# Optimization experiments

Hardware: AMD Instinct MI355X
Metric: run time of the kernel (lower is better)

The kernel has to match this reference:

```python
import jax, jax.numpy as jnp
import numpy as np

N_GRID = 512
B = 4
NUM_VIEWS = 4
EPS = 1e-6


def _build_mesh(n):
    # grid mesh with |v| in (0, 0.9] so log(|v|/(1-|v|)) is finite and sign(v) != 0
    xs = np.linspace(-0.9, 0.9, n, dtype=np.float32)  # 512 points -> no exact zero
    X, Y = np.meshgrid(xs, xs, indexing='ij')
    Z = 0.1 * np.abs(np.sin(3.0 * X) * np.cos(3.0 * Y)) + 0.01
    V = np.stack([X, Y, Z], -1).reshape(-1, 3).astype(np.float32)
    idx = np.arange(n * n).reshape(n, n)
    v00, v01 = idx[:-1, :-1].ravel(), idx[:-1, 1:].ravel()
    v10, v11 = idx[1:, :-1].ravel(), idx[1:, 1:].ravel()
    f1 = np.stack([v00, v10, v01], -1)
    f2 = np.stack([v10, v11, v01], -1)
    F = np.concatenate([f1, f2], 0).astype(np.int64)
    return V, F


def _topology(F, nv):
    # per-face edges + the opposite vertex of each edge within its face
    e = np.concatenate([F[:, [0, 1]], F[:, [1, 2]], F[:, [2, 0]]], 0)
    opp = np.concatenate([F[:, 2], F[:, 0], F[:, 1]], 0)
    key = np.sort(e, axis=1)
    uniq, inv, counts = np.unique(key, axis=0, return_inverse=True, return_counts=True)
    # LaplacianLoss: unique neighbor pairs (matrix assignment dedups), both directions
    src = np.concatenate([uniq[:, 0], uniq[:, 1]]).astype(np.int32)
    dst = np.concatenate([uniq[:, 1], uniq[:, 0]]).astype(np.int32)
    deg = np.bincount(dst, minlength=nv).astype(np.int32)
    # FlattenLoss: edges shared by exactly two faces -> (v0,v1) edge, (v2,v3) opposite verts
    order = np.argsort(inv, kind='stable')
    starts = np.searchsorted(inv[order], np.arange(len(uniq)))
    m2 = counts == 2
    i1 = order[starts[m2]]
    i2 = order[starts[m2] + 1]
    v0s = uniq[m2, 0].astype(np.int32)
    v1s = uniq[m2, 1].astype(np.int32)
    v2s = opp[i1].astype(np.int32)
    v3s = opp[i2].astype(np.int32)
    return src, dst, deg, v0s, v1s, v2s, v3s


def setup_inputs() -> dict:
    key = jax.random.key(0)
    k1, k2, k3 = jax.random.split(key, 3)
    Vt, F = _build_mesh(N_GRID)
    nv = Vt.shape[0]
    src, dst, deg, v0s, v1s, v2s, v3s = _topology(F, nv)
    return {
        'displace': jax.random.normal(k1, (B, nv, 3), jnp.float32) * 0.1,
        'center': jax.random.normal(k2, (B, 1, 3), jnp.float32) * 0.1,
        'texture': jax.random.uniform(k3, (B, nv, 3), jnp.float32),
        'template_vertices': jnp.asarray(Vt)[None],  # [1, V, 3]
        'lap_src': jnp.asarray(src),
        'lap_dst': jnp.asarray(dst),
        'deg': jnp.asarray(deg),
        'v0s': jnp.asarray(v0s),
        'v1s': jnp.asarray(v1s),
        'v2s': jnp.asarray(v2s),
        'v3s': jnp.asarray(v3s),
        'num_views': NUM_VIEWS,
    }


def reference(displace, center, texture, template_vertices, lap_src, lap_dst, deg,
              v0s, v1s, v2s, v3s, num_views):
    nv = template_vertices.shape[1]
    tv = template_vertices  # [1, V, 3]
    # vertex warp (elementwise)
    base = jnp.log(jnp.abs(tv) / (1.0 - jnp.abs(tv)))
    centroid = jnp.tanh(center)  # [B, 1, 3]
    v = jax.nn.sigmoid(base + displace) * jnp.sign(tv)  # [B, V, 3]
    v = jax.nn.relu(v) * (1.0 - centroid) - jax.nn.relu(-v) * (centroid + 1.0)
    v = v + centroid

    # uniform Laplacian loss: Lx = x - mean(neighbors); sum of squares per batch, mean over batch
    inv_deg = 1.0 / deg.astype(v.dtype)

    def lap_one(x):  # x: [V, 3]
        nbr = jax.ops.segment_sum(x[lap_src], lap_dst, num_segments=nv)
        return x - nbr * inv_deg[:, None]

    lx = jax.vmap(lap_one)(v)
    lap_loss = jnp.mean(jnp.sum(lx * lx, axis=(1, 2)))

    # flatten loss over face pairs sharing an edge
    p0, p1, p2, p3 = v[:, v0s], v[:, v1s], v[:, v2s], v[:, v3s]  # [B, P, 3]
    a1 = p1 - p0
    a1l2 = jnp.sum(a1 * a1, -1)
    a1l1 = jnp.sqrt(a1l2 + EPS)

    def _comp(b):
        bl2 = jnp.sum(b * b, -1)
        bl1 = jnp.sqrt(bl2 + EPS)
        ab = jnp.sum(a1 * b, -1)
        cos = ab / (a1l1 * bl1 + EPS)
        sin = jnp.sqrt(1.0 - cos * cos + EPS)
        cb = b - a1 * (ab / (a1l2 + EPS))[..., None]
        return cb, bl1 * sin

    cb1, l1 = _comp(p2 - p0)
    cb2, l2 = _comp(p3 - p0)
    cos = jnp.sum(cb1 * cb2, -1) / (l1 * l2 + EPS)
    flat_loss = jnp.mean(jnp.sum((cos + 1.0) ** 2, axis=1))

    # torch repeat(1, numViews, 1).reshape(numViews*B, V, 3) == tile then reshape
    b = v.shape[0]
    verts_out = jnp.tile(v, (1, num_views, 1)).reshape(num_views * b, nv, 3)
    tex_out = jnp.tile(texture, (1, num_views, 1)).reshape(num_views * b, nv, 3)
    return verts_out, tex_out, lap_loss, flat_loss
```

## Files before the change

kernel.cpp:

```cpp
#include <hip/hip_runtime.h>

#define NGRID 512
#define NV (NGRID * NGRID)
#define NB 4
#define NVIEWS 4
#define FEPS 1e-6f
#define TR 2
#define LDS_ROWS (TR + 2)
#define ROWF (NGRID * 3)
#define LDSF (LDS_ROWS * ROWF)

typedef float fvec4 __attribute__((ext_vector_type(4)));

static constexpr size_t NVF3 = (size_t)NV * 3;
static constexpr size_t VERTS_FLOATS = (size_t)NVIEWS * NB * NVF3;
static constexpr size_t LAP_OFF = 2 * VERTS_FLOATS;
static constexpr size_t FLAT_OFF = LAP_OFF + 1;

__device__ __forceinline__ float frcp(float x)  { return __builtin_amdgcn_rcpf(x); }
__device__ __forceinline__ float fsqrt_(float x){ return __builtin_amdgcn_sqrtf(x); }

__global__ void init_losses(float* __restrict__ out) {
    if (threadIdx.x == 0) {
        out[LAP_OFF] = 0.0f;
        out[FLAT_OFF] = 0.0f;
    }
}

__device__ __forceinline__ float3 ldsP(const float* __restrict__ vs, int lr, int c) {
    const int o = lr * ROWF + c * 3;
    return make_float3(vs[o], vs[o + 1], vs[o + 2]);
}

__device__ __forceinline__ float edge_val(float3 p0, float3 p1, float3 p2, float3 p3) {
    const float a1x = p1.x - p0.x, a1y = p1.y - p0.y, a1z = p1.z - p0.z;
    const float a1l2 = a1x * a1x + a1y * a1y + a1z * a1z;
    const float a1l1 = fsqrt_(a1l2 + FEPS);
    const float inv_a1l2 = frcp(a1l2 + FEPS);

    const float b1x = p2.x - p0.x, b1y = p2.y - p0.y, b1z = p2.z - p0.z;
    const float b1l2 = b1x * b1x + b1y * b1y + b1z * b1z;
    const float b1l1 = fsqrt_(b1l2 + FEPS);
    const float ab1 = a1x * b1x + a1y * b1y + a1z * b1z;
    const float cos1 = ab1 * frcp(a1l1 * b1l1 + FEPS);
    const float sin1 = fsqrt_(1.0f - cos1 * cos1 + FEPS);
    const float f1 = ab1 * inv_a1l2;
    const float cb1x = b1x - a1x * f1, cb1y = b1y - a1y * f1, cb1z = b1z - a1z * f1;
    const float l1 = b1l1 * sin1;

    const float b2x = p3.x - p0.x, b2y = p3.y - p0.y, b2z = p3.z - p0.z;
    const float b2l2 = b2x * b2x + b2y * b2y + b2z * b2z;
    const float b2l1 = fsqrt_(b2l2 + FEPS);
    const float ab2 = a1x * b2x + a1y * b2y + a1z * b2z;
    const float cos2 = ab2 * frcp(a1l1 * b2l1 + FEPS);
    const float sin2 = fsqrt_(1.0f - cos2 * cos2 + FEPS);
    const float f2 = ab2 * inv_a1l2;
    const float cb2x = b2x - a1x * f2, cb2y = b2y - a1y * f2, cb2z = b2z - a1z * f2;
    const float l2 = b2l1 * sin2;

    const float cosd = (cb1x * cb2x + cb1y * cb2y + cb1z * cb2z) * frcp(l1 * l2 + FEPS);
    const float t = cosd + 1.0f;
    return t * t;
}

__global__ __launch_bounds__(256) void mesh_fused_kernel(
    const float* __restrict__ disp, const float* __restrict__ center,
    const float* __restrict__ tex, const float* __restrict__ tv,
    float* __restrict__ out)
{
    __shared__ float vs[LDSF];
    const int tid = threadIdx.x;
    const int b = blockIdx.y;
    const int R0 = blockIdx.x * TR;

    const float c0 = tanhf(center[b * 3 + 0]);
    const float c1 = tanhf(center[b * 3 + 1]);
    const float c2 = tanhf(center[b * 3 + 2]);
    const float carr[3] = {c0, c1, c2};

    {
        const fvec4* __restrict__ tv4 = (const fvec4*)tv;
        const fvec4* __restrict__ d4p = (const fvec4*)(disp + (size_t)b * NVF3);
        fvec4* __restrict__ vs4 = (fvec4*)vs;
        const int start4 = (R0 - 1) * (ROWF / 4);
#pragma unroll
        for (int ss = 0; ss < LDSF / 4 / 256; ++ss) {
            const int ff4 = ss * 256 + tid;
            const int g4 = start4 + ff4;
            if (g4 < 0 || g4 >= (int)(NVF3 / 4)) continue;
            const fvec4 t = tv4[g4];
            const fvec4 d = d4p[g4];
            fvec4 vr;
            int comp = ff4 % 3;
#pragma unroll
            for (int l = 0; l < 4; ++l) {
                const float tvl = t[l];
                const float s = fabsf(tvl);
                const float sgn = (tvl > 0.0f) ? 1.0f : -1.0f;
                const float e = __expf(-d[l]);
                const float sigma = s * frcp(fmaf(1.0f - s, e, s));
                const float c = carr[comp];
                vr[l] = fmaf(sigma, sgn - c, c);
                comp = (comp == 2) ? 0 : comp + 1;
            }
            vs4[ff4] = vr;
        }
    }
    __syncthreads();

    {
        const fvec4* __restrict__ vs4 = (const fvec4*)vs;
        const fvec4* __restrict__ t4p = (const fvec4*)(tex + (size_t)b * NVF3);
        fvec4* __restrict__ out4 = (fvec4*)out;
        const size_t blk4 = NVF3 / 4;
        const int tile_base4 = R0 * (ROWF / 4);
#pragma unroll
        for (int qq = 0; qq < TR * ROWF / 4 / 256; ++qq) {
            const int q = qq * 256 + tid;
            const fvec4 vo = vs4[ROWF / 4 + q];
            const fvec4 tx = __builtin_nontemporal_load(&t4p[tile_base4 + q]);
            const size_t pos4 = (size_t)tile_base4 + q;
#pragma unroll
            for (int view = 0; view < NVIEWS; ++view) {
                const size_t base = (size_t)(b * NVIEWS + view) * blk4;
                __builtin_nontemporal_store(vo, &out4[base + pos4]);
                __builtin_nontemporal_store(tx, &out4[(VERTS_FLOATS / 4) + base + pos4]);
            }
        }
    }

    float lap_sum = 0.0f, flat_sum = 0.0f;
#pragma unroll 1
    for (int it = 0; it < TR * NGRID / 256; ++it) {
        const int idx = it * 256 + tid;
        const int r_off = idx >> 9;
        const int c = idx & (NGRID - 1);
        const int gr = R0 + r_off;
        const int lr = r_off + 1;

        const float3 pc = ldsP(vs, lr, c);

        {
            float sx = 0.f, sy = 0.f, sz = 0.f;
            int deg = 0;
            if (gr > 0)               { float3 p = ldsP(vs, lr - 1, c);     sx += p.x; sy += p.y; sz += p.z; deg++; }
            if (gr < NGRID - 1)       { float3 p = ldsP(vs, lr + 1, c);     sx += p.x; sy += p.y; sz += p.z; deg++; }
            if (c > 0)                { float3 p = ldsP(vs, lr, c - 1);     sx += p.x; sy += p.y; sz += p.z; deg++; }
            if (c < NGRID - 1)        { float3 p = ldsP(vs, lr, c + 1);     sx += p.x; sy += p.y; sz += p.z; deg++; }
            if (gr > 0 && c < NGRID - 1)      { float3 p = ldsP(vs, lr - 1, c + 1); sx += p.x; sy += p.y; sz += p.z; deg++; }
            if (gr < NGRID - 1 && c > 0)      { float3 p = ldsP(vs, lr + 1, c - 1); sx += p.x; sy += p.y; sz += p.z; deg++; }
            const float id = frcp((float)deg);
            const float lx = pc.x - sx * id;
            const float ly = pc.y - sy * id;
            const float lz = pc.z - sz * id;
            lap_sum += lx * lx + ly * ly + lz * lz;
        }

        if (gr < NGRID - 1 && c < NGRID - 1) {
            flat_sum += edge_val(ldsP(vs, lr, c + 1), ldsP(vs, lr + 1, c),
                                 pc,                  ldsP(vs, lr + 1, c + 1));
        }
        if (gr >= 1 && gr < NGRID - 1 && c < NGRID - 1) {
            flat_sum += edge_val(pc, ldsP(vs, lr, c + 1),
                                 ldsP(vs, lr + 1, c), ldsP(vs, lr - 1, c + 1));
        }
        if (gr < NGRID - 1 && c >= 1 && c < NGRID - 1) {
            flat_sum += edge_val(pc, ldsP(vs, lr + 1, c),
                                 ldsP(vs, lr, c + 1), ldsP(vs, lr + 1, c - 1));
        }
    }

#pragma unroll
    for (int off = 32; off > 0; off >>= 1) {
        lap_sum  += __shfl_down(lap_sum, off, 64);
        flat_sum += __shfl_down(flat_sum, off, 64);
    }
    __shared__ float red[8];
    const int lane = tid & 63;
    const int wid = tid >> 6;
    if (lane == 0) { red[wid] = lap_sum; red[4 + wid] = flat_sum; }
    __syncthreads();
    if (tid == 0) {
        const float ls = red[0] + red[1] + red[2] + red[3];
        const float fs = red[4] + red[5] + red[6] + red[7];
        atomicAdd(&out[LAP_OFF],  ls * (1.0f / NB));
        atomicAdd(&out[FLAT_OFF], fs * (1.0f / NB));
    }
}

extern "C" void kernel_launch(void* const* d_in, const int* in_sizes, int n_in,
                              void* d_out, int out_size, void* d_ws, size_t ws_size,
                              hipStream_t stream)
{
    const float* disp   = (const float*)d_in[0];
    const float* center = (const float*)d_in[1];
    const float* tex    = (const float*)d_in[2];
    const float* tv     = (const float*)d_in[3];
    float* out = (float*)d_out;

    init_losses<<<1, 64, 0, stream>>>(out);
    mesh_fused_kernel<<<dim3(NGRID / TR, NB), 256, 0, stream>>>(disp, center, tex, tv, out);
}
```

Before: 177.5 us.

## Pad LDS vertices to float4 and fuse output writes into the load loop

Stores each vertex in LDS as a padded float4 instead of packed float3, so stencil neighbors are read with single 128-bit LDS loads instead of three scalar loads. The loop that replicates vertices and textures to the output is folded into the load/transform loop, writing straight from registers instead of re-reading LDS after a barrier. It also raises the occupancy hint in launch bounds. LDS writes become scattered scalar stores, and the padding increases the LDS footprint; the +1 element covers the trailing out-of-range neighbor read.

```diff
diff --git a/kernel.cpp b/kernel.cpp
--- a/kernel.cpp
+++ b/kernel.cpp
@@ -8,7 +8,7 @@
 #define TR 2
 #define LDS_ROWS (TR + 2)
 #define ROWF (NGRID * 3)
-#define LDSF (LDS_ROWS * ROWF)
+#define LDSF4 (LDS_ROWS * ROWF / 4)
 
 typedef float fvec4 __attribute__((ext_vector_type(4)));
 
@@ -27,12 +27,7 @@
     }
 }
 
-__device__ __forceinline__ float3 ldsP(const float* __restrict__ vs, int lr, int c) {
-    const int o = lr * ROWF + c * 3;
-    return make_float3(vs[o], vs[o + 1], vs[o + 2]);
-}
-
-__device__ __forceinline__ float edge_val(float3 p0, float3 p1, float3 p2, float3 p3) {
+__device__ __forceinline__ float edge_val(fvec4 p0, fvec4 p1, fvec4 p2, fvec4 p3) {
     const float a1x = p1.x - p0.x, a1y = p1.y - p0.y, a1z = p1.z - p0.z;
     const float a1l2 = a1x * a1x + a1y * a1y + a1z * a1z;
     const float a1l1 = fsqrt_(a1l2 + FEPS);
@@ -63,12 +58,14 @@
     return t * t;
 }
 
-__global__ __launch_bounds__(256) void mesh_fused_kernel(
+__global__ __launch_bounds__(256, 4) void mesh_fused_kernel(
     const float* __restrict__ disp, const float* __restrict__ center,
     const float* __restrict__ tex, const float* __restrict__ tv,
     float* __restrict__ out)
 {
-    __shared__ float vs[LDSF];
+    __shared__ fvec4 vsp[LDS_ROWS * NGRID + 1];
+    float* __restrict__ vs_f = (float*)vsp;
+
     const int tid = threadIdx.x;
     const int b = blockIdx.y;
     const int R0 = blockIdx.x * TR;
@@ -81,53 +78,56 @@
     {
         const fvec4* __restrict__ tv4 = (const fvec4*)tv;
         const fvec4* __restrict__ d4p = (const fvec4*)(disp + (size_t)b * NVF3);
-        fvec4* __restrict__ vs4 = (fvec4*)vs;
-        const int start4 = (R0 - 1) * (ROWF / 4);
-#pragma unroll
-        for (int ss = 0; ss < LDSF / 4 / 256; ++ss) {
-            const int ff4 = ss * 256 + tid;
-            const int g4 = start4 + ff4;
-            if (g4 < 0 || g4 >= (int)(NVF3 / 4)) continue;
-            const fvec4 t = tv4[g4];
-            const fvec4 d = d4p[g4];
-            fvec4 vr;
-            int comp = ff4 % 3;
-#pragma unroll
-            for (int l = 0; l < 4; ++l) {
-                const float tvl = t[l];
-                const float s = fabsf(tvl);
-                const float sgn = (tvl > 0.0f) ? 1.0f : -1.0f;
-                const float e = __expf(-d[l]);
-                const float sigma = s * frcp(fmaf(1.0f - s, e, s));
-                const float c = carr[comp];
-                vr[l] = fmaf(sigma, sgn - c, c);
-                comp = (comp == 2) ? 0 : comp + 1;
-            }
-            vs4[ff4] = vr;
-        }
-    }
-    __syncthreads();
-
-    {
-        const fvec4* __restrict__ vs4 = (const fvec4*)vs;
         const fvec4* __restrict__ t4p = (const fvec4*)(tex + (size_t)b * NVF3);
         fvec4* __restrict__ out4 = (fvec4*)out;
         const size_t blk4 = NVF3 / 4;
-        const int tile_base4 = R0 * (ROWF / 4);
-#pragma unroll
-        for (int qq = 0; qq < TR * ROWF / 4 / 256; ++qq) {
-            const int q = qq * 256 + tid;
-            const fvec4 vo = vs4[ROWF / 4 + q];
-            const fvec4 tx = __builtin_nontemporal_load(&t4p[tile_base4 + q]);
-            const size_t pos4 = (size_t)tile_base4 + q;
-#pragma unroll
-            for (int view = 0; view < NVIEWS; ++view) {
-                const size_t base = (size_t)(b * NVIEWS + view) * blk4;
-                __builtin_nontemporal_store(vo, &out4[base + pos4]);
-                __builtin_nontemporal_store(tx, &out4[(VERTS_FLOATS / 4) + base + pos4]);
+        const int start4 = (R0 - 1) * (ROWF / 4);
+#pragma unroll
+        for (int ss = 0; ss < LDSF4 / 256; ++ss) {
+            const int q = ss * 256 + tid;
+            const int g4 = start4 + q;
+            const int rowq = q / (ROWF / 4);
+            if (g4 >= 0 && g4 < (int)(NVF3 / 4)) {
+                const fvec4 t = tv4[g4];
+                const fvec4 d = d4p[g4];
+                fvec4 vr;
+                int comp = q % 3;
+#pragma unroll
+                for (int l = 0; l < 4; ++l) {
+                    const float tvl = t[l];
+                    const float s = fabsf(tvl);
+                    const float sgn = (tvl > 0.0f) ? 1.0f : -1.0f;
+                    const float e = __expf(-d[l]);
+                    const float sigma = s * frcp(fmaf(1.0f - s, e, s));
+                    const float c = carr[comp];
+                    vr[l] = fmaf(sigma, sgn - c, c);
+                    comp = (comp == 2) ? 0 : comp + 1;
+                }
+                {
+                    const int k = q / 3;
+                    const int cc = q - 3 * k;
+                    int point = 4 * k + cc;
+                    int comp2 = cc;
+#pragma unroll
+                    for (int l = 0; l < 4; ++l) {
+                        vs_f[point * 4 + comp2] = vr[l];
+                        comp2++;
+                        if (comp2 == 3) { comp2 = 0; point++; }
+                    }
+                }
+                if (rowq >= 1 && rowq <= TR) {
+                    const fvec4 tx = __builtin_nontemporal_load(&t4p[g4]);
+#pragma unroll
+                    for (int view = 0; view < NVIEWS; ++view) {
+                        const size_t base = (size_t)(b * NVIEWS + view) * blk4;
+                        __builtin_nontemporal_store(vr, &out4[base + g4]);
+                        __builtin_nontemporal_store(tx, &out4[(VERTS_FLOATS / 4) + base + g4]);
+                    }
+                }
             }
         }
     }
+    __syncthreads();
 
     float lap_sum = 0.0f, flat_sum = 0.0f;
 #pragma unroll 1
@@ -137,36 +137,41 @@
         const int c = idx & (NGRID - 1);
         const int gr = R0 + r_off;
         const int lr = r_off + 1;
-
-        const float3 pc = ldsP(vs, lr, c);
+        const int base = lr * NGRID + c;
+
+        const fvec4 C  = vsp[base];
+        const fvec4 Nn = vsp[base - NGRID];
+        const fvec4 S  = vsp[base + NGRID];
+        const fvec4 W  = vsp[base - 1];
+        const fvec4 E  = vsp[base + 1];
+        const fvec4 NE = vsp[base - NGRID + 1];
+        const fvec4 SW = vsp[base + NGRID - 1];
+        const fvec4 SE = vsp[base + NGRID + 1];
 
         {
             float sx = 0.f, sy = 0.f, sz = 0.f;
             int deg = 0;
-            if (gr > 0)               { float3 p = ldsP(vs, lr - 1, c);     sx += p.x; sy += p.y; sz += p.z; deg++; }
-            if (gr < NGRID - 1)       { float3 p = ldsP(vs, lr + 1, c);     sx += p.x; sy += p.y; sz += p.z; deg++; }
-            if (c > 0)                { float3 p = ldsP(vs, lr, c - 1);     sx += p.x; sy += p.y; sz += p.z; deg++; }
-            if (c < NGRID - 1)        { float3 p = ldsP(vs, lr, c + 1);     sx += p.x; sy += p.y; sz += p.z; deg++; }
-            if (gr > 0 && c < NGRID - 1)      { float3 p = ldsP(vs, lr - 1, c + 1); sx += p.x; sy += p.y; sz += p.z; deg++; }
-            if (gr < NGRID - 1 && c > 0)      { float3 p = ldsP(vs, lr + 1, c - 1); sx += p.x; sy += p.y; sz += p.z; deg++; }
+            if (gr > 0)               { sx += Nn.x; sy += Nn.y; sz += Nn.z; deg++; }
+            if (gr < NGRID - 1)       { sx += S.x;  sy += S.y;  sz += S.z;  deg++; }
+            if (c > 0)                { sx += W.x;  sy += W.y;  sz += W.z;  deg++; }
+            if (c < NGRID - 1)        { sx += E.x;  sy += E.y;  sz += E.z;  deg++; }
+            if (gr > 0 && c < NGRID - 1)      { sx += NE.x; sy += NE.y; sz += NE.z; deg++; }
+            if (gr < NGRID - 1 && c > 0)      { sx += SW.x; sy += SW.y; sz += SW.z; deg++; }
             const float id = frcp((float)deg);
-            const float lx = pc.x - sx * id;
-            const float ly = pc.y - sy * id;
-            const float lz = pc.z - sz * id;
+            const float lx = C.x - sx * id;
+            const float ly = C.y - sy * id;
+            const float lz = C.z - sz * id;
             lap_sum += lx * lx + ly * ly + lz * lz;
         }
 
         if (gr < NGRID - 1 && c < NGRID - 1) {
-            flat_sum += edge_val(ldsP(vs, lr, c + 1), ldsP(vs, lr + 1, c),
-                                 pc,                  ldsP(vs, lr + 1, c + 1));
+            flat_sum += edge_val(E, S, C, SE);
         }
         if (gr >= 1 && gr < NGRID - 1 && c < NGRID - 1) {
-            flat_sum += edge_val(pc, ldsP(vs, lr, c + 1),
-                                 ldsP(vs, lr + 1, c), ldsP(vs, lr - 1, c + 1));
+            flat_sum += edge_val(C, E, S, NE);
         }
         if (gr < NGRID - 1 && c >= 1 && c < NGRID - 1) {
-            flat_sum += edge_val(pc, ldsP(vs, lr + 1, c),
-                                 ldsP(vs, lr, c + 1), ldsP(vs, lr + 1, c - 1));
+            flat_sum += edge_val(C, S, E, SW);
         }
     }
 
```

After: 187.0 us. +5.4%, slower.

## Split fused kernel into streaming transform/store kernel and separate loss kernel

Applied to the files above, without the earlier changes.

Moves the replicated vertex and texture output stores out of the LDS-tiled loss kernel into a dedicated grid-stride streaming kernel, which also zeroes the loss accumulators. The loss kernel then only builds the LDS tile and reduces. This separates the bandwidth-bound store phase from the compute phase so each can run at its own occupancy. In exchange it reads displacement and template twice and recomputes the sigmoid transform in both kernels.

```diff
diff --git a/kernel.cpp b/kernel.cpp
--- a/kernel.cpp
+++ b/kernel.cpp
@@ -13,6 +13,7 @@
 typedef float fvec4 __attribute__((ext_vector_type(4)));
 
 static constexpr size_t NVF3 = (size_t)NV * 3;
+static constexpr size_t BLK4 = NVF3 / 4;
 static constexpr size_t VERTS_FLOATS = (size_t)NVIEWS * NB * NVF3;
 static constexpr size_t LAP_OFF = 2 * VERTS_FLOATS;
 static constexpr size_t FLAT_OFF = LAP_OFF + 1;
@@ -20,10 +21,54 @@
 __device__ __forceinline__ float frcp(float x)  { return __builtin_amdgcn_rcpf(x); }
 __device__ __forceinline__ float fsqrt_(float x){ return __builtin_amdgcn_sqrtf(x); }
 
-__global__ void init_losses(float* __restrict__ out) {
-    if (threadIdx.x == 0) {
+__device__ __forceinline__ float xform(float tvl, float d, float c) {
+    const float s = fabsf(tvl);
+    const float sgn = (tvl > 0.0f) ? 1.0f : -1.0f;
+    const float e = __expf(-d);
+    const float sigma = s * frcp(fmaf(1.0f - s, e, s));
+    return fmaf(sigma, sgn - c, c);
+}
+
+__global__ __launch_bounds__(256) void transform_store_kernel(
+    const float* __restrict__ disp, const float* __restrict__ center,
+    const float* __restrict__ tex, const float* __restrict__ tv,
+    float* __restrict__ out)
+{
+    const int tid = threadIdx.x;
+    const int b = blockIdx.y;
+
+    if (blockIdx.x == 0 && b == 0 && tid == 0) {
         out[LAP_OFF] = 0.0f;
         out[FLAT_OFF] = 0.0f;
+    }
+
+    const float c0 = tanhf(center[b * 3 + 0]);
+    const float c1 = tanhf(center[b * 3 + 1]);
+    const float c2 = tanhf(center[b * 3 + 2]);
+    const float carr[3] = {c0, c1, c2};
+
+    const fvec4* __restrict__ tv4 = (const fvec4*)tv;
+    const fvec4* __restrict__ d4p = (const fvec4*)(disp + (size_t)b * NVF3);
+    const fvec4* __restrict__ t4p = (const fvec4*)(tex + (size_t)b * NVF3);
+    fvec4* __restrict__ out4 = (fvec4*)out;
+
+    for (int g4 = blockIdx.x * 256 + tid; g4 < (int)BLK4; g4 += gridDim.x * 256) {
+        const fvec4 t = tv4[g4];
+        const fvec4 d = d4p[g4];
+        const fvec4 tx = __builtin_nontemporal_load(&t4p[g4]);
+        fvec4 vr;
+        int comp = g4 % 3;
+#pragma unroll
+        for (int l = 0; l < 4; ++l) {
+            vr[l] = xform(t[l], d[l], carr[comp]);
+            comp = (comp == 2) ? 0 : comp + 1;
+        }
+#pragma unroll
+        for (int view = 0; view < NVIEWS; ++view) {
+            const size_t base = (size_t)(b * NVIEWS + view) * BLK4;
+            __builtin_nontemporal_store(vr, &out4[base + g4]);
+            __builtin_nontemporal_store(tx, &out4[(VERTS_FLOATS / 4) + base + g4]);
+        }
     }
 }
 
@@ -63,10 +108,9 @@
     return t * t;
 }
 
-__global__ __launch_bounds__(256) void mesh_fused_kernel(
+__global__ __launch_bounds__(256) void loss_kernel(
     const float* __restrict__ disp, const float* __restrict__ center,
-    const float* __restrict__ tex, const float* __restrict__ tv,
-    float* __restrict__ out)
+    const float* __restrict__ tv, float* __restrict__ out)
 {
     __shared__ float vs[LDSF];
     const int tid = threadIdx.x;
@@ -94,40 +138,13 @@
             int comp = ff4 % 3;
 #pragma unroll
             for (int l = 0; l < 4; ++l) {
-                const float tvl = t[l];
-                const float s = fabsf(tvl);
-                const float sgn = (tvl > 0.0f) ? 1.0f : -1.0f;
-                const float e = __expf(-d[l]);
-                const float sigma = s * frcp(fmaf(1.0f - s, e, s));
-                const float c = carr[comp];
-                vr[l] = fmaf(sigma, sgn - c, c);
+                vr[l] = xform(t[l], d[l], carr[comp]);
                 comp = (comp == 2) ? 0 : comp + 1;
             }
             vs4[ff4] = vr;
         }
     }
     __syncthreads();
-
-    {
-        const fvec4* __restrict__ vs4 = (const fvec4*)vs;
-        const fvec4* __restrict__ t4p = (const fvec4*)(tex + (size_t)b * NVF3);
-        fvec4* __restrict__ out4 = (fvec4*)out;
-        const size_t blk4 = NVF3 / 4;
-        const int tile_base4 = R0 * (ROWF / 4);
-#pragma unroll
-        for (int qq = 0; qq < TR * ROWF / 4 / 256; ++qq) {
-            const int q = qq * 256 + tid;
-            const fvec4 vo = vs4[ROWF / 4 + q];
-            const fvec4 tx = __builtin_nontemporal_load(&t4p[tile_base4 + q]);
-            const size_t pos4 = (size_t)tile_base4 + q;
-#pragma unroll
-            for (int view = 0; view < NVIEWS; ++view) {
-                const size_t base = (size_t)(b * NVIEWS + view) * blk4;
-                __builtin_nontemporal_store(vo, &out4[base + pos4]);
-                __builtin_nontemporal_store(tx, &out4[(VERTS_FLOATS / 4) + base + pos4]);
-            }
-        }
-    }
 
     float lap_sum = 0.0f, flat_sum = 0.0f;
 #pragma unroll 1
@@ -198,6 +215,6 @@
     const float* tv     = (const float*)d_in[3];
     float* out = (float*)d_out;
 
-    init_losses<<<1, 64, 0, stream>>>(out);
-    mesh_fused_kernel<<<dim3(NGRID / TR, NB), 256, 0, stream>>>(disp, center, tex, tv, out);
-}
+    transform_store_kernel<<<dim3(512, NB), 256, 0, stream>>>(disp, center, tex, tv, out);
+    loss_kernel<<<dim3(NGRID / TR, NB), 256, 0, stream>>>(disp, center, tv, out);
+}
```

Result: slower. 194.7 us (+9.7%).
